# Performance work log

Hardware: AMD Instinct MI355X
Metric: run time of the kernel (lower is better)

## Reference

```python
import jax, jax.numpy as jnp
import numpy as np

B, N, M, K, D = 8, 100000, 2048, 32, 128
EPS = 1e-5


def setup_inputs() -> dict:
    key = jax.random.key(0)
    ks = jax.random.split(key, 10)
    return dict(
        point_feat=jax.random.normal(ks[0], (B, N, D), jnp.float32),
        point_xyz=jax.random.normal(ks[1], (B, N, 3), jnp.float32),
        supernode_xyz=jax.random.normal(ks[2], (B, M, 3), jnp.float32),
        neighbor_idx=jax.random.randint(ks[3], (B, M, K), 0, N),
        neighbor_mask=jax.random.randint(ks[4], (B, M, K), 0, 2).astype(bool),
        supernode_init_feat=jax.random.normal(ks[5], (B, M, D), jnp.float32),
        task_emb=jax.random.normal(ks[6], (B, D), jnp.float32),
        W1=jax.random.normal(ks[7], (D + 4, D), jnp.float32) * 0.05,
        b1=jnp.zeros((D,), jnp.float32),
        W2=jax.random.normal(ks[8], (D, D), jnp.float32) * 0.05,
        b2=jnp.zeros((D,), jnp.float32),
        Wf=jax.random.normal(ks[9], (D, 2 * D), jnp.float32) * 0.02,  # FiLM head (identity-ish init)
        bf=jnp.zeros((2 * D,), jnp.float32),
        ln_g=jnp.ones((D,), jnp.float32),
        ln_b=jnp.zeros((D,), jnp.float32),
    )


def reference(point_feat, point_xyz, supernode_xyz, neighbor_idx, neighbor_mask,
              supernode_init_feat, task_emb, W1, b1, W2, b2, Wf, bf, ln_g, ln_b):
    # batched neighbor gather: [B,M,K] indices into [B,N,*]
    gather = jax.vmap(lambda feats, idx: feats[idx])
    neigh_feat = gather(point_feat, neighbor_idx)            # [B,M,K,D]
    neigh_xyz = gather(point_xyz, neighbor_idx)              # [B,M,K,3]
    rel = neigh_xyz - supernode_xyz[:, :, None, :]           # [B,M,K,3]
    dist = jnp.linalg.norm(rel, axis=-1, keepdims=True)      # [B,M,K,1]
    x = jnp.concatenate([neigh_feat, rel, dist], axis=-1)    # [B,M,K,D+4]
    msg = jax.nn.silu(x @ W1 + b1) @ W2 + b2                 # [B,M,K,D]
    # masked mean over neighbors, denom clamped to >= 1
    mask_f = neighbor_mask.astype(msg.dtype)[..., None]      # [B,M,K,1]
    agg = (msg * mask_f).sum(axis=2) / jnp.maximum(mask_f.sum(axis=2), 1.0)  # [B,M,D]
    # task FiLM: x * (1 + gamma) + beta
    gamma, beta = jnp.split(task_emb @ Wf + bf, 2, axis=-1)  # each [B,D]
    agg = agg * (1.0 + gamma[:, None, :]) + beta[:, None, :]
    # residual + LayerNorm
    h = supernode_init_feat + agg
    mu = h.mean(axis=-1, keepdims=True)
    var = ((h - mu) ** 2).mean(axis=-1, keepdims=True)
    return (h - mu) * jax.lax.rsqrt(var + EPS) * ln_g + ln_b
```

## Files before the change

kernel.cpp:

```cpp
#include <hip/hip_runtime.h>
#include <hip/hip_bf16.h>

#define B_ 8
#define N_ 100000
#define M_ 2048
#define K_ 32
#define D_ 128
#define KPL 168
#define KL2 136
#define EPS_ 1e-5f

typedef __attribute__((ext_vector_type(8))) short bf16x8;
typedef __attribute__((ext_vector_type(4))) float f32x4;

__device__ __forceinline__ short f2bf(float f) {
    unsigned int u = __builtin_bit_cast(unsigned int, f);
    u += 0x7fffu + ((u >> 16) & 1u);
    return (short)(u >> 16);
}

__global__ __launch_bounds__(256) void prep_kernel(
    const float* __restrict__ W1, const float* __restrict__ b1,
    const float* __restrict__ W2,
    const float* __restrict__ task_emb, const float* __restrict__ Wf,
    const float* __restrict__ bfv,
    short* __restrict__ w1t, short* __restrict__ w2t, float* __restrict__ gb)
{
    if (blockIdx.x == 0) {
        for (int e = threadIdx.x; e < 128 * KPL; e += 256) {
            const int n = e / KPL;
            const int k = e - n * KPL;
            float v = 0.f;
            if (k < 132) v = W1[k * 128 + n];
            else if (k == 132) v = b1[n];
            w1t[e] = f2bf(v);
        }
    } else if (blockIdx.x == 1) {
        for (int e = threadIdx.x; e < 128 * KL2; e += 256) {
            const int n = e / KL2;
            const int k = e - n * KL2;
            w2t[e] = f2bf(k < 128 ? W2[k * 128 + n] : 0.f);
        }
    } else {
        const int b = blockIdx.x - 2;
        const int col = threadIdx.x;
        float acc = bfv[col];
        for (int i = 0; i < 128; ++i) acc += task_emb[b * 128 + i] * Wf[i * 256 + col];
        gb[b * 256 + col] = acc;
    }
}

__global__ __launch_bounds__(256) void msg_kernel(
    const float* __restrict__ point_feat,
    const float* __restrict__ point_xyz,
    const float* __restrict__ supernode_xyz,
    const int*   __restrict__ nidx,
    const int*   __restrict__ nmask,
    const short* __restrict__ w1t,
    float* __restrict__ agg_out,
    float* __restrict__ cflag)
{
    __shared__ short sw[128 * KPL];
    {
        const uint2* src = (const uint2*)w1t;
        uint2* dst = (uint2*)sw;
        #pragma unroll
        for (int i = 0; i < 21; ++i) dst[threadIdx.x + i * 256] = src[threadIdx.x + i * 256];
    }
    __syncthreads();

    const int lane = threadIdx.x & 63;
    const int wave = threadIdx.x >> 6;
    const int sm = blockIdx.x * 4 + wave;
    const int b  = sm >> 11;
    const int c  = lane & 15;
    const int q  = lane >> 4;
    const long base_bm = (long)sm * K_;

    const int idx0 = nidx[base_bm + c];
    const int idx1 = nidx[base_bm + 16 + c];

    const bool mv = (lane < K_) && (nmask[base_bm + lane] != 0);
    const unsigned long long bal = __ballot(mv);
    const int cnt = __popcll(bal);
    const float inv_d = 1.0f / (float)(cnt > 0 ? cnt : 1);
    const bool v0 = (bal >> c) & 1ULL;
    const bool v1 = (bal >> (16 + c)) & 1ULL;

    const float* sxp = supernode_xyz + (long)sm * 3;
    const float sx = sxp[0], sy = sxp[1], sz = sxp[2];

    union U { bf16x8 v; short s[8]; };

    U a4[2];
    {
        const int idxs[2] = { idx0, idx1 };
        const bool vs[2] = { v0, v1 };
        #pragma unroll
        for (int tt = 0; tt < 2; ++tt) {
            U u;
            #pragma unroll
            for (int jj = 0; jj < 8; ++jj) u.s[jj] = 0;
            if (q == 0 && vs[tt]) {
                const float* p = point_xyz + ((long)b * N_ + idxs[tt]) * 3;
                const float rx = p[0] - sx, ry = p[1] - sy, rz = p[2] - sz;
                const float dd = sqrtf(rx * rx + ry * ry + rz * rz);
                u.s[0] = f2bf(rx); u.s[1] = f2bf(ry); u.s[2] = f2bf(rz);
                u.s[3] = f2bf(dd); u.s[4] = f2bf(1.0f);
            }
            a4[tt] = u;
        }
    }

    const f32x4 zero = { 0.f, 0.f, 0.f, 0.f };
    f32x4 acc[2][8];
    #pragma unroll
    for (int mt = 0; mt < 2; ++mt)
        #pragma unroll
        for (int nt = 0; nt < 8; ++nt) acc[mt][nt] = zero;

    const float* featb = point_feat + (long)b * N_ * D_;
    const float* prow0 = featb + (long)idx0 * D_ + q * 8;
    const float* prow1 = featb + (long)idx1 * D_ + q * 8;
    const short* wb = sw + c * KPL + q * 8;

    #pragma unroll
    for (int ks = 0; ks < 4; ++ks) {
        bf16x8 bfr[8];
        #pragma unroll
        for (int nt = 0; nt < 8; ++nt)
            bfr[nt] = *reinterpret_cast<const bf16x8*>(wb + nt * 16 * KPL + ks * 32);
        U ua0 = {}, ua1 = {};
        if (v0) {
            const f32x4 x0 = *reinterpret_cast<const f32x4*>(prow0 + ks * 32);
            const f32x4 x1 = *reinterpret_cast<const f32x4*>(prow0 + ks * 32 + 4);
            #pragma unroll
            for (int jj = 0; jj < 4; ++jj) { ua0.s[jj] = f2bf(x0[jj]); ua0.s[4 + jj] = f2bf(x1[jj]); }
        }
        if (v1) {
            const f32x4 y0 = *reinterpret_cast<const f32x4*>(prow1 + ks * 32);
            const f32x4 y1 = *reinterpret_cast<const f32x4*>(prow1 + ks * 32 + 4);
            #pragma unroll
            for (int jj = 0; jj < 4; ++jj) { ua1.s[jj] = f2bf(y0[jj]); ua1.s[4 + jj] = f2bf(y1[jj]); }
        }
        #pragma unroll
        for (int nt = 0; nt < 8; ++nt) {
            acc[0][nt] = __builtin_amdgcn_mfma_f32_16x16x32_bf16(ua0.v, bfr[nt], acc[0][nt], 0, 0, 0);
            acc[1][nt] = __builtin_amdgcn_mfma_f32_16x16x32_bf16(ua1.v, bfr[nt], acc[1][nt], 0, 0, 0);
        }
    }
    #pragma unroll
    for (int nt = 0; nt < 8; ++nt) {
        const bf16x8 bfr = *reinterpret_cast<const bf16x8*>(wb + nt * 16 * KPL + 4 * 32);
        acc[0][nt] = __builtin_amdgcn_mfma_f32_16x16x32_bf16(a4[0].v, bfr, acc[0][nt], 0, 0, 0);
        acc[1][nt] = __builtin_amdgcn_mfma_f32_16x16x32_bf16(a4[1].v, bfr, acc[1][nt], 0, 0, 0);
    }

    #pragma unroll
    for (int nt = 0; nt < 8; ++nt) {
        float part = 0.f;
        #pragma unroll
        for (int mt = 0; mt < 2; ++mt) {
            #pragma unroll
            for (int r = 0; r < 4; ++r) {
                const int row = mt * 16 + q * 4 + r;
                const float v = acc[mt][nt][r];
                const float s = v / (1.0f + __expf(-v));
                part += ((bal >> row) & 1ULL) ? s : 0.0f;
            }
        }
        part += __shfl_xor(part, 16);
        part += __shfl_xor(part, 32);
        if (q == 0) agg_out[(long)sm * D_ + nt * 16 + c] = part * inv_d;
    }
    if (lane == 0) cflag[sm] = (cnt > 0) ? 1.0f : 0.0f;
}

__global__ __launch_bounds__(256) void out_kernel(
    float* __restrict__ inout,
    const short* __restrict__ w2t,
    const float* __restrict__ b2,
    const float* __restrict__ cflag,
    const float* __restrict__ gb,
    const float* __restrict__ init_feat,
    const float* __restrict__ ln_g,
    const float* __restrict__ ln_b)
{
    __shared__ short sw[128 * KL2];
    {
        const uint2* src = (const uint2*)w2t;
        uint2* dst = (uint2*)sw;
        #pragma unroll
        for (int i = 0; i < 17; ++i) dst[threadIdx.x + i * 256] = src[threadIdx.x + i * 256];
    }
    __syncthreads();

    const int lane = threadIdx.x & 63;
    const int wave = threadIdx.x >> 6;
    const int s0 = blockIdx.x * 64 + wave * 16;
    const int b  = s0 >> 11;
    const int c  = lane & 15;
    const int q  = lane >> 4;

    union U { bf16x8 v; short s[8]; };
    const f32x4 zero = { 0.f, 0.f, 0.f, 0.f };
    f32x4 acc[8];
    #pragma unroll
    for (int nt = 0; nt < 8; ++nt) acc[nt] = zero;

    const float* arow = inout + (long)(s0 + c) * D_ + q * 8;
    const short* wb = sw + c * KL2 + q * 8;

    #pragma unroll
    for (int ks = 0; ks < 4; ++ks) {
        U ua;
        {
            const f32x4 x0 = *reinterpret_cast<const f32x4*>(arow + ks * 32);
            const f32x4 x1 = *reinterpret_cast<const f32x4*>(arow + ks * 32 + 4);
            #pragma unroll
            for (int jj = 0; jj < 4; ++jj) { ua.s[jj] = f2bf(x0[jj]); ua.s[4 + jj] = f2bf(x1[jj]); }
        }
        #pragma unroll
        for (int nt = 0; nt < 8; ++nt) {
            const bf16x8 bfr = *reinterpret_cast<const bf16x8*>(wb + nt * 16 * KL2 + ks * 32);
            acc[nt] = __builtin_amdgcn_mfma_f32_16x16x32_bf16(ua.v, bfr, acc[nt], 0, 0, 0);
        }
    }

    float gv[8], bev[8], b2v[8], lgv[8], lbv[8];
    #pragma unroll
    for (int nt = 0; nt < 8; ++nt) {
        const int col = nt * 16 + c;
        gv[nt]  = gb[b * 256 + col];
        bev[nt] = gb[b * 256 + 128 + col];
        b2v[nt] = b2[col];
        lgv[nt] = ln_g[col];
        lbv[nt] = ln_b[col];
    }

    #pragma unroll
    for (int r = 0; r < 4; ++r) {
        const int row = s0 + q * 4 + r;
        const float cf = cflag[row];
        float h[8];
        float s1 = 0.f, s2 = 0.f;
        #pragma unroll
        for (int nt = 0; nt < 8; ++nt) {
            const float msgv = acc[nt][r] + cf * b2v[nt];
            const float v = msgv * (1.f + gv[nt]) + bev[nt];
            const float hh = init_feat[(long)row * D_ + nt * 16 + c] + v;
            h[nt] = hh; s1 += hh; s2 += hh * hh;
        }
        #pragma unroll
        for (int off = 1; off < 16; off <<= 1) {
            s1 += __shfl_xor(s1, off);
            s2 += __shfl_xor(s2, off);
        }
        const float mu = s1 * (1.f / 128.f);
        const float var = s2 * (1.f / 128.f) - mu * mu;
        const float rs = rsqrtf(var + EPS_);
        #pragma unroll
        for (int nt = 0; nt < 8; ++nt)
            inout[(long)row * D_ + nt * 16 + c] = (h[nt] - mu) * rs * lgv[nt] + lbv[nt];
    }
}

extern "C" void kernel_launch(void* const* d_in, const int* in_sizes, int n_in,
                              void* d_out, int out_size, void* d_ws, size_t ws_size,
                              hipStream_t stream) {
    const float* point_feat     = (const float*)d_in[0];
    const float* point_xyz      = (const float*)d_in[1];
    const float* supernode_xyz  = (const float*)d_in[2];
    const int*   neighbor_idx   = (const int*)d_in[3];
    const int*   neighbor_mask  = (const int*)d_in[4];
    const float* supernode_init = (const float*)d_in[5];
    const float* task_emb       = (const float*)d_in[6];
    const float* W1             = (const float*)d_in[7];
    const float* b1             = (const float*)d_in[8];
    const float* W2             = (const float*)d_in[9];
    const float* b2             = (const float*)d_in[10];
    const float* Wf             = (const float*)d_in[11];
    const float* bfv            = (const float*)d_in[12];
    const float* ln_g           = (const float*)d_in[13];
    const float* ln_b           = (const float*)d_in[14];

    char* ws = (char*)d_ws;
    short* w1t  = (short*)ws;
    short* w2t  = (short*)(ws + 44032);
    float* gb   = (float*)(ws + 78848);
    float* cfl  = (float*)(ws + 87040);
    float* out  = (float*)d_out;

    prep_kernel<<<10, 256, 0, stream>>>(W1, b1, W2, task_emb, Wf, bfv, w1t, w2t, gb);
    msg_kernel<<<(B_ * M_) / 4, 256, 0, stream>>>(point_feat, point_xyz, supernode_xyz,
                                                  neighbor_idx, neighbor_mask, w1t, out, cfl);
    out_kernel<<<(B_ * M_) / 64, 256, 0, stream>>>(out, w2t, b2, cfl, gb,
                                                   supernode_init, ln_g, ln_b);
}
```

Before: 590.7 us.

## Issue neighbor gathers before weight staging; truncate bf16 packing; parallelize prep

The message kernel now issues all neighbor feature and xyz gathers up front, before copying W1 into shared memory, so the global gather latency overlaps the weight staging and barrier. Masked neighbors read row 0 instead of branching, keeping loads uniform. Float-to-bf16 conversion for activations switches from round-to-nearest to a single byte-permute truncation, which slightly changes numerics. The prep kernel spreads the weight transposes over 32 blocks with coalesced reads. Holding 64 floats of prefetched data per lane raises register pressure.

```diff
diff --git a/kernel.cpp b/kernel.cpp
--- a/kernel.cpp
+++ b/kernel.cpp
@@ -18,6 +18,11 @@
     u += 0x7fffu + ((u >> 16) & 1u);
     return (short)(u >> 16);
 }
+__device__ __forceinline__ unsigned int pack_bf2(float lo, float hi) {
+    return __builtin_amdgcn_perm(__builtin_bit_cast(unsigned int, hi),
+                                 __builtin_bit_cast(unsigned int, lo),
+                                 0x07060302u);
+}
 
 __global__ __launch_bounds__(256) void prep_kernel(
     const float* __restrict__ W1, const float* __restrict__ b1,
@@ -26,27 +31,35 @@
     const float* __restrict__ bfv,
     short* __restrict__ w1t, short* __restrict__ w2t, float* __restrict__ gb)
 {
-    if (blockIdx.x == 0) {
-        for (int e = threadIdx.x; e < 128 * KPL; e += 256) {
-            const int n = e / KPL;
-            const int k = e - n * KPL;
-            float v = 0.f;
-            if (k < 132) v = W1[k * 128 + n];
-            else if (k == 132) v = b1[n];
-            w1t[e] = f2bf(v);
-        }
-    } else if (blockIdx.x == 1) {
-        for (int e = threadIdx.x; e < 128 * KL2; e += 256) {
-            const int n = e / KL2;
-            const int k = e - n * KL2;
-            w2t[e] = f2bf(k < 128 ? W2[k * 128 + n] : 0.f);
+    const int t = threadIdx.x;
+    if (blockIdx.x < 16) {
+        const int bid = blockIdx.x;
+        #pragma unroll
+        for (int it = 0; it < 6; ++it) {
+            const int e = bid * 1344 + it * 256 + t;
+            if (e < (bid + 1) * 1344 && e < KPL * 128) {
+                const int k = e >> 7, n = e & 127;
+                float v = 0.f;
+                if (k < 132) v = W1[k * 128 + n];
+                else if (k == 132) v = b1[n];
+                w1t[n * KPL + k] = f2bf(v);
+            }
+        }
+    } else if (blockIdx.x < 32) {
+        const int bid = blockIdx.x - 16;
+        #pragma unroll
+        for (int it = 0; it < 5; ++it) {
+            const int e = bid * 1088 + it * 256 + t;
+            if (e < (bid + 1) * 1088 && e < KL2 * 128) {
+                const int k = e >> 7, n = e & 127;
+                w2t[n * KL2 + k] = f2bf(k < 128 ? W2[k * 128 + n] : 0.f);
+            }
         }
     } else {
-        const int b = blockIdx.x - 2;
-        const int col = threadIdx.x;
-        float acc = bfv[col];
-        for (int i = 0; i < 128; ++i) acc += task_emb[b * 128 + i] * Wf[i * 256 + col];
-        gb[b * 256 + col] = acc;
+        const int b = blockIdx.x - 32;
+        float acc = bfv[t];
+        for (int i = 0; i < 128; ++i) acc += task_emb[b * 128 + i] * Wf[i * 256 + t];
+        gb[b * 256 + t] = acc;
     }
 }
 
@@ -61,13 +74,6 @@
     float* __restrict__ cflag)
 {
     __shared__ short sw[128 * KPL];
-    {
-        const uint2* src = (const uint2*)w1t;
-        uint2* dst = (uint2*)sw;
-        #pragma unroll
-        for (int i = 0; i < 21; ++i) dst[threadIdx.x + i * 256] = src[threadIdx.x + i * 256];
-    }
-    __syncthreads();
 
     const int lane = threadIdx.x & 63;
     const int wave = threadIdx.x >> 6;
@@ -79,37 +85,68 @@
 
     const int idx0 = nidx[base_bm + c];
     const int idx1 = nidx[base_bm + 16 + c];
-
     const bool mv = (lane < K_) && (nmask[base_bm + lane] != 0);
     const unsigned long long bal = __ballot(mv);
     const int cnt = __popcll(bal);
     const float inv_d = 1.0f / (float)(cnt > 0 ? cnt : 1);
     const bool v0 = (bal >> c) & 1ULL;
     const bool v1 = (bal >> (16 + c)) & 1ULL;
+    const int ridx0 = v0 ? idx0 : 0;
+    const int ridx1 = v1 ? idx1 : 0;
+
+    const float* featb = point_feat + (long)b * N_ * D_;
+    const float* prow0 = featb + (long)ridx0 * D_ + q * 8;
+    const float* prow1 = featb + (long)ridx1 * D_ + q * 8;
+    f32x4 r0[8], r1[8];
+    #pragma unroll
+    for (int ks = 0; ks < 4; ++ks) {
+        r0[2 * ks]     = *reinterpret_cast<const f32x4*>(prow0 + ks * 32);
+        r0[2 * ks + 1] = *reinterpret_cast<const f32x4*>(prow0 + ks * 32 + 4);
+        r1[2 * ks]     = *reinterpret_cast<const f32x4*>(prow1 + ks * 32);
+        r1[2 * ks + 1] = *reinterpret_cast<const f32x4*>(prow1 + ks * 32 + 4);
+    }
 
     const float* sxp = supernode_xyz + (long)sm * 3;
     const float sx = sxp[0], sy = sxp[1], sz = sxp[2];
-
-    union U { bf16x8 v; short s[8]; };
-
+    const float* p0 = point_xyz + ((long)b * N_ + ridx0) * 3;
+    const float* p1 = point_xyz + ((long)b * N_ + ridx1) * 3;
+    const float rx0 = p0[0] - sx, ry0 = p0[1] - sy, rz0 = p0[2] - sz;
+    const float rx1 = p1[0] - sx, ry1 = p1[1] - sy, rz1 = p1[2] - sz;
+    const float dd0 = sqrtf(rx0 * rx0 + ry0 * ry0 + rz0 * rz0);
+    const float dd1 = sqrtf(rx1 * rx1 + ry1 * ry1 + rz1 * rz1);
+
+    union U { bf16x8 v; short s[8]; unsigned int u[4]; };
     U a4[2];
+    #pragma unroll
+    for (int jj = 0; jj < 8; ++jj) { a4[0].s[jj] = 0; a4[1].s[jj] = 0; }
+    if (q == 0) {
+        a4[0].s[0] = f2bf(rx0); a4[0].s[1] = f2bf(ry0); a4[0].s[2] = f2bf(rz0);
+        a4[0].s[3] = f2bf(dd0); a4[0].s[4] = f2bf(1.0f);
+        a4[1].s[0] = f2bf(rx1); a4[1].s[1] = f2bf(ry1); a4[1].s[2] = f2bf(rz1);
+        a4[1].s[3] = f2bf(dd1); a4[1].s[4] = f2bf(1.0f);
+    }
+
     {
-        const int idxs[2] = { idx0, idx1 };
-        const bool vs[2] = { v0, v1 };
-        #pragma unroll
-        for (int tt = 0; tt < 2; ++tt) {
-            U u;
-            #pragma unroll
-            for (int jj = 0; jj < 8; ++jj) u.s[jj] = 0;
-            if (q == 0 && vs[tt]) {
-                const float* p = point_xyz + ((long)b * N_ + idxs[tt]) * 3;
-                const float rx = p[0] - sx, ry = p[1] - sy, rz = p[2] - sz;
-                const float dd = sqrtf(rx * rx + ry * ry + rz * rz);
-                u.s[0] = f2bf(rx); u.s[1] = f2bf(ry); u.s[2] = f2bf(rz);
-                u.s[3] = f2bf(dd); u.s[4] = f2bf(1.0f);
-            }
-            a4[tt] = u;
-        }
+        const uint2* src = (const uint2*)w1t;
+        uint2* dst = (uint2*)sw;
+        #pragma unroll
+        for (int i = 0; i < 21; ++i) dst[threadIdx.x + i * 256] = src[threadIdx.x + i * 256];
+    }
+    __syncthreads();
+
+    U a0[4], a1[4];
+    #pragma unroll
+    for (int ks = 0; ks < 4; ++ks) {
+        const f32x4 x0 = r0[2 * ks], x1 = r0[2 * ks + 1];
+        const f32x4 y0 = r1[2 * ks], y1 = r1[2 * ks + 1];
+        a0[ks].u[0] = pack_bf2(x0[0], x0[1]);
+        a0[ks].u[1] = pack_bf2(x0[2], x0[3]);
+        a0[ks].u[2] = pack_bf2(x1[0], x1[1]);
+        a0[ks].u[3] = pack_bf2(x1[2], x1[3]);
+        a1[ks].u[0] = pack_bf2(y0[0], y0[1]);
+        a1[ks].u[1] = pack_bf2(y0[2], y0[3]);
+        a1[ks].u[2] = pack_bf2(y1[0], y1[1]);
+        a1[ks].u[3] = pack_bf2(y1[2], y1[3]);
     }
 
     const f32x4 zero = { 0.f, 0.f, 0.f, 0.f };
@@ -119,34 +156,14 @@
         #pragma unroll
         for (int nt = 0; nt < 8; ++nt) acc[mt][nt] = zero;
 
-    const float* featb = point_feat + (long)b * N_ * D_;
-    const float* prow0 = featb + (long)idx0 * D_ + q * 8;
-    const float* prow1 = featb + (long)idx1 * D_ + q * 8;
     const short* wb = sw + c * KPL + q * 8;
-
     #pragma unroll
     for (int ks = 0; ks < 4; ++ks) {
-        bf16x8 bfr[8];
-        #pragma unroll
-        for (int nt = 0; nt < 8; ++nt)
-            bfr[nt] = *reinterpret_cast<const bf16x8*>(wb + nt * 16 * KPL + ks * 32);
-        U ua0 = {}, ua1 = {};
-        if (v0) {
-            const f32x4 x0 = *reinterpret_cast<const f32x4*>(prow0 + ks * 32);
-            const f32x4 x1 = *reinterpret_cast<const f32x4*>(prow0 + ks * 32 + 4);
-            #pragma unroll
-            for (int jj = 0; jj < 4; ++jj) { ua0.s[jj] = f2bf(x0[jj]); ua0.s[4 + jj] = f2bf(x1[jj]); }
-        }
-        if (v1) {
-            const f32x4 y0 = *reinterpret_cast<const f32x4*>(prow1 + ks * 32);
-            const f32x4 y1 = *reinterpret_cast<const f32x4*>(prow1 + ks * 32 + 4);
-            #pragma unroll
-            for (int jj = 0; jj < 4; ++jj) { ua1.s[jj] = f2bf(y0[jj]); ua1.s[4 + jj] = f2bf(y1[jj]); }
-        }
         #pragma unroll
         for (int nt = 0; nt < 8; ++nt) {
-            acc[0][nt] = __builtin_amdgcn_mfma_f32_16x16x32_bf16(ua0.v, bfr[nt], acc[0][nt], 0, 0, 0);
-            acc[1][nt] = __builtin_amdgcn_mfma_f32_16x16x32_bf16(ua1.v, bfr[nt], acc[1][nt], 0, 0, 0);
+            const bf16x8 bfr = *reinterpret_cast<const bf16x8*>(wb + nt * 16 * KPL + ks * 32);
+            acc[0][nt] = __builtin_amdgcn_mfma_f32_16x16x32_bf16(a0[ks].v, bfr, acc[0][nt], 0, 0, 0);
+            acc[1][nt] = __builtin_amdgcn_mfma_f32_16x16x32_bf16(a1[ks].v, bfr, acc[1][nt], 0, 0, 0);
         }
     }
     #pragma unroll
@@ -202,7 +219,7 @@
     const int c  = lane & 15;
     const int q  = lane >> 4;
 
-    union U { bf16x8 v; short s[8]; };
+    union U { bf16x8 v; short s[8]; unsigned int u[4]; };
     const f32x4 zero = { 0.f, 0.f, 0.f, 0.f };
     f32x4 acc[8];
     #pragma unroll
@@ -217,8 +234,10 @@
         {
             const f32x4 x0 = *reinterpret_cast<const f32x4*>(arow + ks * 32);
             const f32x4 x1 = *reinterpret_cast<const f32x4*>(arow + ks * 32 + 4);
-            #pragma unroll
-            for (int jj = 0; jj < 4; ++jj) { ua.s[jj] = f2bf(x0[jj]); ua.s[4 + jj] = f2bf(x1[jj]); }
+            ua.u[0] = pack_bf2(x0[0], x0[1]);
+            ua.u[1] = pack_bf2(x0[2], x0[3]);
+            ua.u[2] = pack_bf2(x1[0], x1[1]);
+            ua.u[3] = pack_bf2(x1[2], x1[3]);
         }
         #pragma unroll
         for (int nt = 0; nt < 8; ++nt) {
@@ -291,7 +310,7 @@
     float* cfl  = (float*)(ws + 87040);
     float* out  = (float*)d_out;
 
-    prep_kernel<<<10, 256, 0, stream>>>(W1, b1, W2, task_emb, Wf, bfv, w1t, w2t, gb);
+    prep_kernel<<<40, 256, 0, stream>>>(W1, b1, W2, task_emb, Wf, bfv, w1t, w2t, gb);
     msg_kernel<<<(B_ * M_) / 4, 256, 0, stream>>>(point_feat, point_xyz, supernode_xyz,
                                                   neighbor_idx, neighbor_mask, w1t, out, cfl);
     out_kernel<<<(B_ * M_) / 64, 256, 0, stream>>>(out, w2t, b2, cfl, gb,
```

After: 570.9 us. 3.3% less time.
